# Performance work log

Hardware: AMD Instinct MI355X
Metric: run time of the kernel (lower is better)

## Reference

```python
import jax, jax.numpy as jnp
import numpy as np

EPS = 1e-12  # torch F.normalize eps

def _l2norm(v, axis):
    n = jnp.sqrt(jnp.sum(v * v, axis=axis, keepdims=True))
    return v / jnp.maximum(n, EPS)

def setup_inputs() -> dict:
    key = jax.random.key(0)
    k1, k2 = jax.random.split(key)
    B, N, D, K = 8, 2048, 128, 64
    x = jax.random.normal(k1, (B, N, D), dtype=jnp.float32)
    std1 = 1.0 / np.sqrt(K * D)
    centroids = jax.random.uniform(k2, (K, D), dtype=jnp.float32, minval=-std1, maxval=std1)
    return {"x": x, "centroids": centroids}

def reference(x, centroids):
    # x: [B, N, D], centroids: [K, D]
    B, N, D = x.shape
    K = centroids.shape[0]
    xn = _l2norm(x, axis=-1)                       # descriptor-wise L2 normalize
    res = xn[:, :, None, :] - centroids[None, None]  # [B, N, K, D]
    dist = jnp.sum(res * res, axis=-1)             # [B, N, K] squared distances
    assign = jax.nn.softmax(dist, axis=-1)         # softmax over clusters (NOTE: positive distances, as in source)
    vlad = jnp.einsum('bnk,bnkd->bkd', assign, res)  # weighted residual sum over N
    vlad = _l2norm(vlad, axis=2)                   # intra-normalization per cluster
    vlad = vlad.reshape(B, K * D)
    vlad = _l2norm(vlad, axis=1)                   # global L2 normalize
    return vlad
```

## Files before the change

### kernel.cpp

```cpp
#include <hip/hip_runtime.h>
#include <math.h>

#define BB 8
#define NN 2048
#define DD 128
#define KK 64
#define PP 128
#define NPB (NN / PP)

__global__ __launch_bounds__(256, 4) void netvlad_k1(
    const float* __restrict__ x, const float* __restrict__ cent,
    float* __restrict__ part_acc, float* __restrict__ part_sA)
{
    const int b    = blockIdx.x >> 7;
    const int p    = blockIdx.x & 127;
    const int t    = threadIdx.x;
    const int kq   = t >> 3;
    const int pr   = t & 7;
    const int dbase = pr * 16;
    const int wave = t >> 6;
    const int lane = t & 63;
    const int half = (t >> 5) & 1;
    const int hl   = t & 31;

    __shared__ float xn[8][DD];
    __shared__ float eL[8][KK];
    __shared__ float rsum[8];

    int off[4];
    #pragma unroll
    for (int jj = 0; jj < 4; ++jj) off[jj] = dbase + (((jj + pr) & 3) << 2);

    float4 cA[4], cB[4];
    float cn2a = 0.f, cn2b = 0.f;
    #pragma unroll
    for (int jj = 0; jj < 4; ++jj) {
        cA[jj] = *(const float4*)(cent + (2 * kq) * DD + off[jj]);
        cB[jj] = *(const float4*)(cent + (2 * kq + 1) * DD + off[jj]);
        cn2a += cA[jj].x*cA[jj].x + cA[jj].y*cA[jj].y + cA[jj].z*cA[jj].z + cA[jj].w*cA[jj].w;
        cn2b += cB[jj].x*cB[jj].x + cB[jj].y*cB[jj].y + cB[jj].z*cB[jj].z + cB[jj].w*cB[jj].w;
    }
    #pragma unroll
    for (int m = 1; m < 8; m <<= 1) {
        cn2a += __shfl_xor(cn2a, m);
        cn2b += __shfl_xor(cn2b, m);
    }

    float4 acc0[4], acc1[4];
    #pragma unroll
    for (int jj = 0; jj < 4; ++jj) {
        acc0[jj] = make_float4(0.f, 0.f, 0.f, 0.f);
        acc1[jj] = make_float4(0.f, 0.f, 0.f, 0.f);
    }
    float sA0 = 0.f, sA1 = 0.f;

    const float* xb = x + ((size_t)b * NN + (size_t)p * NPB) * DD;

    for (int it = 0; it < NPB / 8; ++it) {
        __syncthreads();

        {
            const int i = wave * 2 + half;
            const float* xp = xb + (size_t)(it * 8 + i) * DD + hl * 4;
            float4 v = *(const float4*)xp;
            float ss = v.x*v.x + v.y*v.y + v.z*v.z + v.w*v.w;
            #pragma unroll
            for (int m = 1; m < 32; m <<= 1) ss += __shfl_xor(ss, m);
            const float rn = 1.0f / fmaxf(sqrtf(ss), 1e-12f);
            *(float4*)(&xn[i][hl * 4]) = make_float4(v.x*rn, v.y*rn, v.z*rn, v.w*rn);
        }
        __syncthreads();

        float e0[8], e1[8];
        #pragma unroll
        for (int i = 0; i < 8; ++i) {
            float S0 = 0.f, S1 = 0.f;
            #pragma unroll
            for (int jj = 0; jj < 4; ++jj) {
                float4 v = *(const float4*)(&xn[i][off[jj]]);
                S0 += v.x*cA[jj].x + v.y*cA[jj].y + v.z*cA[jj].z + v.w*cA[jj].w;
                S1 += v.x*cB[jj].x + v.y*cB[jj].y + v.z*cB[jj].z + v.w*cB[jj].w;
            }
            #pragma unroll
            for (int m = 1; m < 8; m <<= 1) {
                S0 += __shfl_xor(S0, m);
                S1 += __shfl_xor(S1, m);
            }
            e0[i] = __expf(cn2a - 2.f * S0);
            e1[i] = __expf(cn2b - 2.f * S1);
            if (pr == 0) *(float2*)(&eL[i][2 * kq]) = make_float2(e0[i], e1[i]);
        }
        __syncthreads();

        #pragma unroll
        for (int rep = 0; rep < 2; ++rep) {
            const int i = wave * 2 + rep;
            float e = eL[i][lane];
            #pragma unroll
            for (int m = 1; m < 64; m <<= 1) e += __shfl_xor(e, m);
            if (lane == 0) rsum[i] = 1.0f / e;
        }
        __syncthreads();

        #pragma unroll
        for (int i = 0; i < 8; ++i) {
            const float r = rsum[i];
            const float a0 = e0[i] * r, a1 = e1[i] * r;
            sA0 += a0; sA1 += a1;
            #pragma unroll
            for (int jj = 0; jj < 4; ++jj) {
                float4 v = *(const float4*)(&xn[i][off[jj]]);
                acc0[jj].x += a0*v.x; acc0[jj].y += a0*v.y; acc0[jj].z += a0*v.z; acc0[jj].w += a0*v.w;
                acc1[jj].x += a1*v.x; acc1[jj].y += a1*v.y; acc1[jj].z += a1*v.z; acc1[jj].w += a1*v.w;
            }
        }
    }

    const size_t base = (size_t)(b * PP + p) * KK * DD;
    #pragma unroll
    for (int jj = 0; jj < 4; ++jj) {
        *(float4*)(part_acc + base + (2 * kq) * DD + off[jj])     = acc0[jj];
        *(float4*)(part_acc + base + (2 * kq + 1) * DD + off[jj]) = acc1[jj];
    }
    if (pr == 0) {
        part_sA[(b * PP + p) * KK + 2 * kq]     = sA0;
        part_sA[(b * PP + p) * KK + 2 * kq + 1] = sA1;
    }
}

__global__ __launch_bounds__(128) void netvlad_k2(
    const float* __restrict__ cent, const float* __restrict__ part_acc,
    const float* __restrict__ part_sA, float* __restrict__ out)
{
    const int b  = blockIdx.x >> 6;
    const int k  = blockIdx.x & 63;
    const int t  = threadIdx.x;
    const int d4 = t & 31;
    const int ps = t >> 5;

    __shared__ float sAL[2];
    {
        float sA = part_sA[(b * PP + t) * KK + k];
        #pragma unroll
        for (int m = 1; m < 64; m <<= 1) sA += __shfl_xor(sA, m);
        if ((t & 63) == 0) sAL[t >> 6] = sA;
    }

    float4 acc = make_float4(0.f, 0.f, 0.f, 0.f);
    const float* base = part_acc + ((size_t)(b * PP) * KK + k) * DD + d4 * 4;
    #pragma unroll 8
    for (int pp = 0; pp < 32; ++pp) {
        const float4 v = *(const float4*)(base + (size_t)(ps * 32 + pp) * KK * DD);
        acc.x += v.x; acc.y += v.y; acc.z += v.z; acc.w += v.w;
    }

    __shared__ float4 red[4][32];
    red[ps][d4] = acc;
    __syncthreads();
    const float sAt = sAL[0] + sAL[1];

    if (t < 32) {
        float4 v = red[0][t];
        #pragma unroll
        for (int s = 1; s < 4; ++s) {
            v.x += red[s][t].x; v.y += red[s][t].y;
            v.z += red[s][t].z; v.w += red[s][t].w;
        }
        const float4 c = *(const float4*)(cent + k * DD + t * 4);
        v.x -= c.x * sAt; v.y -= c.y * sAt; v.z -= c.z * sAt; v.w -= c.w * sAt;

        float ss = v.x*v.x + v.y*v.y + v.z*v.z + v.w*v.w;
        #pragma unroll
        for (int m = 1; m < 32; m <<= 1) ss += __shfl_xor(ss, m);
        const float rn = 0.125f / fmaxf(sqrtf(ss), 1e-12f);
        v.x *= rn; v.y *= rn; v.z *= rn; v.w *= rn;
        *(float4*)(out + ((size_t)b * KK + k) * DD + t * 4) = v;
    }
}

extern "C" void kernel_launch(void* const* d_in, const int* in_sizes, int n_in,
                              void* d_out, int out_size, void* d_ws, size_t ws_size,
                              hipStream_t stream) {
    const float* x    = (const float*)d_in[0];
    const float* cent = (const float*)d_in[1];
    float* out = (float*)d_out;

    char* ws = (char*)d_ws;
    float* part_sA  = (float*)ws;
    float* part_acc = (float*)(ws + (1 << 19));

    netvlad_k1<<<dim3(BB * PP), dim3(256), 0, stream>>>(x, cent, part_acc, part_sA);
    netvlad_k2<<<dim3(BB * KK), dim3(128), 0, stream>>>(cent, part_acc, part_sA, out);
}
```

Measured before the change: 100.2 us.

## Load all 16 rows per block at once and reduce softmax sums via shuffles

Each block now loads and normalizes all 16 of its descriptor rows in a single pass instead of two iterations of 8 rows, and the global x loads are issued before the centroid loads. The softmax denominator is partly reduced with cross-lane shuffles inside each wave, and only the per-wave partials go through shared memory. This cuts the block barriers from eight to two and removes the separate reduction pass over shared memory. In exchange, more e0/e1 values stay live in registers (16 each), which may raise register pressure under the launch bound of 4 blocks.

```diff
diff --git a/kernel.cpp b/kernel.cpp
--- a/kernel.cpp
+++ b/kernel.cpp
@@ -19,17 +19,18 @@
     const int pr   = t & 7;
     const int dbase = pr * 16;
     const int wave = t >> 6;
-    const int lane = t & 63;
-    const int half = (t >> 5) & 1;
-    const int hl   = t & 31;
 
-    __shared__ float xn[8][DD];
-    __shared__ float eL[8][KK];
-    __shared__ float rsum[8];
+    __shared__ __align__(16) float xs[NPB][DD];
+    __shared__ __align__(16) float sL[NPB][4];
 
     int off[4];
     #pragma unroll
     for (int jj = 0; jj < 4; ++jj) off[jj] = dbase + (((jj + pr) & 3) << 2);
+
+    const int i0 = t >> 4, tl = t & 15;
+    const float* xr = x + ((size_t)b * NN + (size_t)p * NPB + i0) * DD;
+    float4 v0 = *(const float4*)(xr + tl * 4);
+    float4 v1 = *(const float4*)(xr + 64 + tl * 4);
 
     float4 cA[4], cB[4];
     float cn2a = 0.f, cn2b = 0.f;
@@ -46,6 +47,43 @@
         cn2b += __shfl_xor(cn2b, m);
     }
 
+    {
+        float ss = v0.x*v0.x + v0.y*v0.y + v0.z*v0.z + v0.w*v0.w
+                 + v1.x*v1.x + v1.y*v1.y + v1.z*v1.z + v1.w*v1.w;
+        #pragma unroll
+        for (int m = 1; m < 16; m <<= 1) ss += __shfl_xor(ss, m);
+        const float rn = 1.0f / fmaxf(sqrtf(ss), 1e-12f);
+        v0.x *= rn; v0.y *= rn; v0.z *= rn; v0.w *= rn;
+        v1.x *= rn; v1.y *= rn; v1.z *= rn; v1.w *= rn;
+        *(float4*)(&xs[i0][tl * 4])      = v0;
+        *(float4*)(&xs[i0][64 + tl * 4]) = v1;
+    }
+    __syncthreads();
+
+    float e0[NPB], e1[NPB];
+    #pragma unroll
+    for (int i = 0; i < NPB; ++i) {
+        float S0 = 0.f, S1 = 0.f;
+        #pragma unroll
+        for (int jj = 0; jj < 4; ++jj) {
+            float4 v = *(const float4*)(&xs[i][off[jj]]);
+            S0 += v.x*cA[jj].x + v.y*cA[jj].y + v.z*cA[jj].z + v.w*cA[jj].w;
+            S1 += v.x*cB[jj].x + v.y*cB[jj].y + v.z*cB[jj].z + v.w*cB[jj].w;
+        }
+        #pragma unroll
+        for (int m = 1; m < 8; m <<= 1) {
+            S0 += __shfl_xor(S0, m);
+            S1 += __shfl_xor(S1, m);
+        }
+        e0[i] = __expf(cn2a - 2.f * S0);
+        e1[i] = __expf(cn2b - 2.f * S1);
+        float es = e0[i] + e1[i];
+        #pragma unroll
+        for (int m = 8; m < 64; m <<= 1) es += __shfl_xor(es, m);
+        if ((t & 63) == 0) sL[i][wave] = es;
+    }
+    __syncthreads();
+
     float4 acc0[4], acc1[4];
     #pragma unroll
     for (int jj = 0; jj < 4; ++jj) {
@@ -53,66 +91,17 @@
         acc1[jj] = make_float4(0.f, 0.f, 0.f, 0.f);
     }
     float sA0 = 0.f, sA1 = 0.f;
-
-    const float* xb = x + ((size_t)b * NN + (size_t)p * NPB) * DD;
-
-    for (int it = 0; it < NPB / 8; ++it) {
-        __syncthreads();
-
-        {
-            const int i = wave * 2 + half;
-            const float* xp = xb + (size_t)(it * 8 + i) * DD + hl * 4;
-            float4 v = *(const float4*)xp;
-            float ss = v.x*v.x + v.y*v.y + v.z*v.z + v.w*v.w;
-            #pragma unroll
-            for (int m = 1; m < 32; m <<= 1) ss += __shfl_xor(ss, m);
-            const float rn = 1.0f / fmaxf(sqrtf(ss), 1e-12f);
-            *(float4*)(&xn[i][hl * 4]) = make_float4(v.x*rn, v.y*rn, v.z*rn, v.w*rn);
-        }
-        __syncthreads();
-
-        float e0[8], e1[8];
+    #pragma unroll
+    for (int i = 0; i < NPB; ++i) {
+        const float4 s4 = *(const float4*)(&sL[i][0]);
+        const float rs = 1.0f / (s4.x + s4.y + s4.z + s4.w);
+        const float a0 = e0[i] * rs, a1 = e1[i] * rs;
+        sA0 += a0; sA1 += a1;
         #pragma unroll
-        for (int i = 0; i < 8; ++i) {
-            float S0 = 0.f, S1 = 0.f;
-            #pragma unroll
-            for (int jj = 0; jj < 4; ++jj) {
-                float4 v = *(const float4*)(&xn[i][off[jj]]);
-                S0 += v.x*cA[jj].x + v.y*cA[jj].y + v.z*cA[jj].z + v.w*cA[jj].w;
-                S1 += v.x*cB[jj].x + v.y*cB[jj].y + v.z*cB[jj].z + v.w*cB[jj].w;
-            }
-            #pragma unroll
-            for (int m = 1; m < 8; m <<= 1) {
-                S0 += __shfl_xor(S0, m);
-                S1 += __shfl_xor(S1, m);
-            }
-            e0[i] = __expf(cn2a - 2.f * S0);
-            e1[i] = __expf(cn2b - 2.f * S1);
-            if (pr == 0) *(float2*)(&eL[i][2 * kq]) = make_float2(e0[i], e1[i]);
-        }
-        __syncthreads();
-
-        #pragma unroll
-        for (int rep = 0; rep < 2; ++rep) {
-            const int i = wave * 2 + rep;
-            float e = eL[i][lane];
-            #pragma unroll
-            for (int m = 1; m < 64; m <<= 1) e += __shfl_xor(e, m);
-            if (lane == 0) rsum[i] = 1.0f / e;
-        }
-        __syncthreads();
-
-        #pragma unroll
-        for (int i = 0; i < 8; ++i) {
-            const float r = rsum[i];
-            const float a0 = e0[i] * r, a1 = e1[i] * r;
-            sA0 += a0; sA1 += a1;
-            #pragma unroll
-            for (int jj = 0; jj < 4; ++jj) {
-                float4 v = *(const float4*)(&xn[i][off[jj]]);
-                acc0[jj].x += a0*v.x; acc0[jj].y += a0*v.y; acc0[jj].z += a0*v.z; acc0[jj].w += a0*v.w;
-                acc1[jj].x += a1*v.x; acc1[jj].y += a1*v.y; acc1[jj].z += a1*v.z; acc1[jj].w += a1*v.w;
-            }
+        for (int jj = 0; jj < 4; ++jj) {
+            float4 v = *(const float4*)(&xs[i][off[jj]]);
+            acc0[jj].x += a0*v.x; acc0[jj].y += a0*v.y; acc0[jj].z += a0*v.z; acc0[jj].w += a0*v.w;
+            acc1[jj].x += a1*v.x; acc1[jj].y += a1*v.y; acc1[jj].z += a1*v.z; acc1[jj].w += a1*v.w;
         }
     }
 
```

New measurement: 92.58 us. -7.6%, faster.
